# Kernel tuning notes

Hardware: AMD Instinct MI355X
Metric: run time of the kernel (lower is better)

## Reference

```python
import jax, jax.numpy as jnp
import numpy as np

N_EMBD = 768
N_HEAD = 12
HEAD_DIM = N_EMBD // N_HEAD


def setup_inputs() -> dict:
    key = jax.random.key(0)
    k1, k2, k3 = jax.random.split(key, 3)
    x = jax.random.normal(k1, (2, 2048, N_EMBD), dtype=jnp.float32)
    # Dense kernels (no bias), scaled like Glorot-ish init
    w_qkv = jax.random.normal(k2, (N_EMBD, 3 * N_EMBD), dtype=jnp.float32) * (1.0 / np.sqrt(N_EMBD))
    w_proj = jax.random.normal(k3, (N_EMBD, N_EMBD), dtype=jnp.float32) * (1.0 / np.sqrt(N_EMBD))
    return {"x": x, "w_qkv": w_qkv, "w_proj": w_proj}


def reference(x, w_qkv, w_proj):
    b, t, _ = x.shape
    qkv = x @ w_qkv                                  # [b, t, 3*n_embd]
    q, k, v = jnp.split(qkv, 3, axis=-1)
    def split_heads(z):
        return z.reshape(b, t, N_HEAD, HEAD_DIM).transpose(0, 2, 1, 3)  # [b, h, t, d]
    q, k, v = split_heads(q), split_heads(k), split_heads(v)
    scale = jnp.float32(HEAD_DIM) ** -0.5
    att = jnp.einsum('bhqd,bhkd->bhqk', q, k) * scale  # [b, h, t, t]
    # lower-triangular causal mask, additive -1e9 on masked (future) positions
    mask = jnp.tril(jnp.ones((t, t), dtype=jnp.float32))
    att = att + (1.0 - mask)[None, None, :, :] * jnp.float32(-1e9)
    att = jax.nn.softmax(att, axis=-1)
    out = jnp.einsum('bhqk,bhkd->bhqd', att, v)      # [b, h, t, d]
    out = out.transpose(0, 2, 1, 3).reshape(b, t, N_EMBD)
    return out @ w_proj
```

## Files before the change

kernel.cpp:

```cpp
#include <hip/hip_runtime.h>

#define T_SEQ   2048
#define EMBD    768
#define N_HEAD  12
#define HDIM    64
#define BATCH   2

typedef float f32x4 __attribute__((ext_vector_type(4)));
typedef short bf16x8 __attribute__((ext_vector_type(8)));
typedef unsigned short u16;
typedef unsigned int u32;
typedef u16 u16x4 __attribute__((ext_vector_type(4)));

#define MFMA_BF16(a, b, c) __builtin_amdgcn_mfma_f32_16x16x32_bf16((a), (b), (c), 0, 0, 0)

__device__ __forceinline__ u16 f2bf(float f) {
    union { float f; unsigned u; } v; v.f = f;
    unsigned r = v.u + 0x7fffu + ((v.u >> 16) & 1u);
    return (u16)(r >> 16);
}

__device__ __forceinline__ u32 pack2(float hi, float lo) {
    union { float f; u32 u; } a, b;
    a.f = hi; b.f = lo;
    return __builtin_amdgcn_perm(a.u, b.u, 0x07060302u);
}

__device__ __forceinline__ void gload_lds16(const u16* g, u16* l) {
    __builtin_amdgcn_global_load_lds(
        (const __attribute__((address_space(1))) u32*)g,
        (__attribute__((address_space(3))) u32*)l, 16, 0, 0);
}

__global__ __launch_bounds__(256) void prep_kernel(
    const float* __restrict__ x, const float* __restrict__ wq,
    const float* __restrict__ wp, u16* __restrict__ xb,
    u16* __restrict__ wqT, u16* __restrict__ wpT)
{
    const int bid = blockIdx.x;
    const int tid = threadIdx.x;
    if (bid < 1536) {
        const int i = bid * 2048 + tid * 8;
        const float4 f0 = *(const float4*)&x[i];
        const float4 f1 = *(const float4*)&x[i + 4];
        bf16x8 r;
        r[0] = (short)f2bf(f0.x); r[1] = (short)f2bf(f0.y);
        r[2] = (short)f2bf(f0.z); r[3] = (short)f2bf(f0.w);
        r[4] = (short)f2bf(f1.x); r[5] = (short)f2bf(f1.y);
        r[6] = (short)f2bf(f1.z); r[7] = (short)f2bf(f1.w);
        *(bf16x8*)&xb[i] = r;
        return;
    }
    __shared__ float tile[32][33];
    const float* W; u16* Wt; int N, t;
    if (bid < 3264) { W = wq; Wt = wqT; N = 2304; t = bid - 1536; }
    else            { W = wp; Wt = wpT; N = 768;  t = bid - 3264; }
    const int ntiles = N / 32;
    const int n0 = (t % ntiles) * 32;
    const int k0 = (t / ntiles) * 32;
    const int c  = tid & 31;
    const int r8 = tid >> 5;
#pragma unroll
    for (int rr = r8; rr < 32; rr += 8)
        tile[rr][c] = W[(size_t)(k0 + rr) * N + n0 + c];
    __syncthreads();
#pragma unroll
    for (int rr = r8; rr < 32; rr += 8)
        Wt[(size_t)(n0 + rr) * 768 + k0 + c] = f2bf(tile[c][rr]);
}

template <int NCOLS, int SCATTER>
__global__ __launch_bounds__(256, 2) void mfma_gemm(
    const u16* __restrict__ A, const u16* __restrict__ Bt,
    float* __restrict__ C, u16* __restrict__ Qo, u16* __restrict__ Ko,
    u16* __restrict__ Vo)
{
    __shared__ u16 As[128 * 64];
    __shared__ u16 Bs[128 * 64];
    const int tid  = threadIdx.x;
    const int lane = tid & 63, wave = tid >> 6;
    const int l15  = lane & 15, quad = lane >> 4;
    const int wy   = wave >> 1, wx = wave & 1;
    const int row0 = blockIdx.y * 128, col0 = blockIdx.x * 128;

    const int sr = lane >> 3;
    const int sc = lane & 7;
    const int g  = sc ^ sr;
    const u16* gA[4]; const u16* gB[4]; u16* lA[4]; u16* lB[4];
#pragma unroll
    for (int i = 0; i < 4; ++i) {
        const int rb = (i * 4 + wave) * 8;
        gA[i] = &A [(size_t)(row0 + rb + sr) * 768 + g * 8];
        gB[i] = &Bt[(size_t)(col0 + rb + sr) * 768 + g * 8];
        lA[i] = &As[rb * 64];
        lB[i] = &Bs[rb * 64];
    }

    f32x4 acc[4][4];
#pragma unroll
    for (int i = 0; i < 4; ++i)
#pragma unroll
        for (int j = 0; j < 4; ++j) acc[i][j] = (f32x4){0.f, 0.f, 0.f, 0.f};

    for (int k0 = 0; k0 < 768; k0 += 64) {
        __syncthreads();
#pragma unroll
        for (int i = 0; i < 4; ++i) gload_lds16(gA[i] + k0, lA[i]);
#pragma unroll
        for (int i = 0; i < 4; ++i) gload_lds16(gB[i] + k0, lB[i]);
        __syncthreads();
        bf16x8 af[4][2], bfr[4][2];
#pragma unroll
        for (int ks = 0; ks < 2; ++ks) {
#pragma unroll
            for (int mt = 0; mt < 4; ++mt)
                af[mt][ks] = *(const bf16x8*)&As[(wy * 64 + mt * 16 + l15) * 64 +
                                                 (((ks * 4 + quad) ^ (l15 & 7)) * 8)];
#pragma unroll
            for (int nt = 0; nt < 4; ++nt)
                bfr[nt][ks] = *(const bf16x8*)&Bs[(wx * 64 + nt * 16 + l15) * 64 +
                                                  (((ks * 4 + quad) ^ (l15 & 7)) * 8)];
        }
#pragma unroll
        for (int ks = 0; ks < 2; ++ks)
#pragma unroll
            for (int mt = 0; mt < 4; ++mt)
#pragma unroll
                for (int nt = 0; nt < 4; ++nt)
                    acc[mt][nt] = MFMA_BF16(af[mt][ks], bfr[nt][ks], acc[mt][nt]);
    }

    const float qscale = 0.18033688f;
#pragma unroll
    for (int mt = 0; mt < 4; ++mt) {
#pragma unroll
        for (int nt = 0; nt < 4; ++nt) {
            const int col = col0 + wx * 64 + nt * 16 + l15;
            if (SCATTER) {
                const int which = col / 768;
                const int hh = (col - which * 768) >> 6;
                const int dd = col & 63;
                if (which == 2) {
                    const int row = row0 + wy * 64 + mt * 16 + quad * 4;
                    const int bb = row >> 11, t0 = row & 2047;
                    u16x4 pk;
#pragma unroll
                    for (int r = 0; r < 4; ++r) pk[r] = f2bf(acc[mt][nt][r]);
                    *(u16x4*)&Vo[((size_t)(bb * N_HEAD + hh) * HDIM + dd) * T_SEQ + t0] = pk;
                } else {
                    u16* dst = (which == 0) ? Qo : Ko;
                    const float sc2 = (which == 0) ? qscale : 1.0f;
                    const size_t hb = (size_t)hh * T_SEQ * HDIM + dd;
#pragma unroll
                    for (int r = 0; r < 4; ++r) {
                        const int row = row0 + wy * 64 + mt * 16 + quad * 4 + r;
                        const int bb = row >> 11, tt = row & 2047;
                        dst[(size_t)bb * N_HEAD * T_SEQ * HDIM + hb + (size_t)tt * HDIM] =
                            f2bf(acc[mt][nt][r] * sc2);
                    }
                }
            } else {
#pragma unroll
                for (int r = 0; r < 4; ++r) {
                    const int row = row0 + wy * 64 + mt * 16 + quad * 4 + r;
                    C[(size_t)row * NCOLS + col] = acc[mt][nt][r];
                }
            }
        }
    }
}

__global__ __launch_bounds__(256, 3) void attn_mfma(
    const u16* __restrict__ Q, const u16* __restrict__ K,
    const u16* __restrict__ Vt, u16* __restrict__ Aout)
{
    __shared__ float Comb[5120];
    u16* PsAll = (u16*)Comb;

    const int tid  = threadIdx.x;
    const int lane = tid & 63, wave = tid >> 6;
    const int l15  = lane & 15, quad = lane >> 4;

    const int f    = blockIdx.x;
    const int slot = f >> 3;
    const int bh   = (f & 7) * 3 + (slot >> 5);
    const int p    = slot & 31;
    const int b    = bh / N_HEAD, h = bh - b * N_HEAD;

    const int j      = (wave < 2) ? (63 - p) : p;
    const int parity = wave & 1;
    const int qb     = j * 32;
    const int nk     = (j >> 1) + 1;
    const size_t base = (size_t)bh * T_SEQ * HDIM;

    bf16x8 qf[2][2];
#pragma unroll
    for (int jq = 0; jq < 2; ++jq)
#pragma unroll
        for (int ks = 0; ks < 2; ++ks)
            qf[jq][ks] = *(const bf16x8*)&Q[base + (size_t)(qb + jq * 16 + l15) * HDIM +
                                            ks * 32 + quad * 8];

    f32x4 o[2][4], l_acc[2];
#pragma unroll
    for (int jq = 0; jq < 2; ++jq) {
        l_acc[jq] = (f32x4){0.f, 0.f, 0.f, 0.f};
#pragma unroll
        for (int nt = 0; nt < 4; ++nt) o[jq][nt] = (f32x4){0.f, 0.f, 0.f, 0.f};
    }

    bf16x8 onesf;
#pragma unroll
    for (int u = 0; u < 8; ++u) onesf[u] = (short)0x3F80;

    u16* myPs = PsAll + wave * 2304;

    for (int kt = parity; kt < nk; kt += 2) {
        const int k0 = kt * 64;

        f32x4 s[4][2];
#pragma unroll
        for (int i = 0; i < 4; ++i)
#pragma unroll
            for (int jq = 0; jq < 2; ++jq) s[i][jq] = (f32x4){0.f, 0.f, 0.f, 0.f};
#pragma unroll
        for (int ks = 0; ks < 2; ++ks) {
            bf16x8 kf[4];
#pragma unroll
            for (int i = 0; i < 4; ++i)
                kf[i] = *(const bf16x8*)&K[base + (size_t)(k0 + i * 16 + l15) * HDIM +
                                           ks * 32 + quad * 8];
#pragma unroll
            for (int i = 0; i < 4; ++i)
#pragma unroll
                for (int jq = 0; jq < 2; ++jq)
                    s[i][jq] = MFMA_BF16(kf[i], qf[jq][ks], s[i][jq]);
        }

        bf16x8 vf[4][2];
#pragma unroll
        for (int nt = 0; nt < 4; ++nt)
#pragma unroll
            for (int ks = 0; ks < 2; ++ks)
                vf[nt][ks] = *(const bf16x8*)&Vt[base + (size_t)(nt * 16 + l15) * T_SEQ +
                                                 k0 + ks * 32 + quad * 8];

#pragma unroll
        for (int i = 0; i < 2; ++i)
#pragma unroll
            for (int jq = 0; jq < 2; ++jq) {
                float pv[4];
                if (k0 + i * 16 + 15 > qb + jq * 16) {
                    const int q = qb + jq * 16 + l15;
#pragma unroll
                    for (int r = 0; r < 4; ++r) {
                        const int key = k0 + i * 16 + quad * 4 + r;
                        pv[r] = exp2f((key > q) ? -1e30f : s[i][jq][r]);
                    }
                } else {
#pragma unroll
                    for (int r = 0; r < 4; ++r) pv[r] = exp2f(s[i][jq][r]);
                }
                uint2 w;
                w.x = pack2(pv[1], pv[0]);
                w.y = pack2(pv[3], pv[2]);
                *(uint2*)&myPs[(jq * 16 + l15) * 72 + i * 16 + quad * 4] = w;
            }

        bf16x8 pa0[2];
#pragma unroll
        for (int jq = 0; jq < 2; ++jq)
            pa0[jq] = *(const bf16x8*)&myPs[(jq * 16 + l15) * 72 + quad * 8];

#pragma unroll
        for (int i = 2; i < 4; ++i)
#pragma unroll
            for (int jq = 0; jq < 2; ++jq) {
                float pv[4];
                if (k0 + i * 16 + 15 > qb + jq * 16) {
                    const int q = qb + jq * 16 + l15;
#pragma unroll
                    for (int r = 0; r < 4; ++r) {
                        const int key = k0 + i * 16 + quad * 4 + r;
                        pv[r] = exp2f((key > q) ? -1e30f : s[i][jq][r]);
                    }
                } else {
#pragma unroll
                    for (int r = 0; r < 4; ++r) pv[r] = exp2f(s[i][jq][r]);
                }
                uint2 w;
                w.x = pack2(pv[1], pv[0]);
                w.y = pack2(pv[3], pv[2]);
                *(uint2*)&myPs[(jq * 16 + l15) * 72 + i * 16 + quad * 4] = w;
            }

#pragma unroll
        for (int jq = 0; jq < 2; ++jq) {
#pragma unroll
            for (int nt = 0; nt < 4; ++nt)
                o[jq][nt] = MFMA_BF16(pa0[jq], vf[nt][0], o[jq][nt]);
            l_acc[jq] = MFMA_BF16(pa0[jq], onesf, l_acc[jq]);
        }

        bf16x8 pa1[2];
#pragma unroll
        for (int jq = 0; jq < 2; ++jq)
            pa1[jq] = *(const bf16x8*)&myPs[(jq * 16 + l15) * 72 + 32 + quad * 8];
#pragma unroll
        for (int jq = 0; jq < 2; ++jq) {
#pragma unroll
            for (int nt = 0; nt < 4; ++nt)
                o[jq][nt] = MFMA_BF16(pa1[jq], vf[nt][1], o[jq][nt]);
            l_acc[jq] = MFMA_BF16(pa1[jq], onesf, l_acc[jq]);
        }
    }

    __syncthreads();
    if (parity == 1) {
        float* R = Comb + (wave >> 1) * 2560;
#pragma unroll
        for (int jq = 0; jq < 2; ++jq) {
#pragma unroll
            for (int nt = 0; nt < 4; ++nt)
#pragma unroll
                for (int r = 0; r < 4; ++r)
                    R[(jq * 16 + nt * 4 + r) * 64 + lane] = o[jq][nt][r];
#pragma unroll
            for (int r = 0; r < 4; ++r)
                R[(32 + jq * 4 + r) * 64 + lane] = l_acc[jq][r];
        }
    }
    __syncthreads();
    if (parity == 0) {
        const float* R = Comb + (wave >> 1) * 2560;
#pragma unroll
        for (int jq = 0; jq < 2; ++jq) {
#pragma unroll
            for (int nt = 0; nt < 4; ++nt)
#pragma unroll
                for (int r = 0; r < 4; ++r)
                    o[jq][nt][r] += R[(jq * 16 + nt * 4 + r) * 64 + lane];
#pragma unroll
            for (int r = 0; r < 4; ++r)
                l_acc[jq][r] += R[(32 + jq * 4 + r) * 64 + lane];
        }
#pragma unroll
        for (int jq = 0; jq < 2; ++jq) {
            f32x4 inv;
#pragma unroll
            for (int r = 0; r < 4; ++r) inv[r] = 1.0f / l_acc[jq][r];
#pragma unroll
            for (int nt = 0; nt < 4; ++nt) {
                const int d = nt * 16 + l15;
#pragma unroll
                for (int r = 0; r < 4; ++r) {
                    const int q = qb + jq * 16 + quad * 4 + r;
                    Aout[(size_t)(b * T_SEQ + q) * EMBD + h * HDIM + d] =
                        f2bf(o[jq][nt][r] * inv[r]);
                }
            }
        }
    }
}

extern "C" void kernel_launch(void* const* d_in, const int* in_sizes, int n_in,
                              void* d_out, int out_size, void* d_ws, size_t ws_size,
                              hipStream_t stream)
{
    (void)in_sizes; (void)n_in; (void)out_size; (void)ws_size;
    const float* x      = (const float*)d_in[0];
    const float* w_qkv  = (const float*)d_in[1];
    const float* w_proj = (const float*)d_in[2];
    float* out = (float*)d_out;

    u16* ws = (u16*)d_ws;
    const size_t NX  = (size_t)BATCH * T_SEQ * EMBD;
    const size_t NWQ = (size_t)EMBD * 3 * EMBD;
    const size_t NWP = (size_t)EMBD * EMBD;
    const size_t SZ  = (size_t)BATCH * N_HEAD * T_SEQ * HDIM;
    u16* xb     = ws;
    u16* wqkvT  = xb + NX;
    u16* wprojT = wqkvT + NWQ;
    u16* Qb     = wprojT + NWP;
    u16* Kb     = Qb + SZ;
    u16* Vtb    = Kb + SZ;
    u16* Ab     = Vtb + SZ;

    dim3 blk(256);
    prep_kernel<<<dim3(3840), blk, 0, stream>>>(x, w_qkv, w_proj, xb, wqkvT, wprojT);

    mfma_gemm<3 * EMBD, 1><<<dim3(3 * EMBD / 128, BATCH * T_SEQ / 128), blk, 0, stream>>>(
        xb, wqkvT, nullptr, Qb, Kb, Vtb);

    attn_mfma<<<dim3(32 * N_HEAD * BATCH), blk, 0, stream>>>(Qb, Kb, Vtb, Ab);

    mfma_gemm<EMBD, 0><<<dim3(EMBD / 128, BATCH * T_SEQ / 128), blk, 0, stream>>>(
        Ab, wprojT, out, nullptr, nullptr, nullptr);
}
```

Before: 163.8 us.

## Prefetch K fragments in attention and use smaller M tile for projection GEMM

```diff
diff --git a/kernel.cpp b/kernel.cpp
--- a/kernel.cpp
+++ b/kernel.cpp
@@ -69,70 +69,74 @@
         Wt[(size_t)(n0 + rr) * 768 + k0 + c] = f2bf(tile[c][rr]);
 }
 
-template <int NCOLS, int SCATTER>
-__global__ __launch_bounds__(256, 2) void mfma_gemm(
+template <int NCOLS, int SCATTER, int TM>
+__global__ __launch_bounds__(256, 3) void mfma_gemm(
     const u16* __restrict__ A, const u16* __restrict__ Bt,
     float* __restrict__ C, u16* __restrict__ Qo, u16* __restrict__ Ko,
     u16* __restrict__ Vo)
 {
-    __shared__ u16 As[128 * 64];
+    constexpr int MT = TM / 32;
+    constexpr int AI = TM / 32;
+    __shared__ u16 As[TM * 64];
     __shared__ u16 Bs[128 * 64];
     const int tid  = threadIdx.x;
     const int lane = tid & 63, wave = tid >> 6;
     const int l15  = lane & 15, quad = lane >> 4;
     const int wy   = wave >> 1, wx = wave & 1;
-    const int row0 = blockIdx.y * 128, col0 = blockIdx.x * 128;
+    const int row0 = blockIdx.y * TM, col0 = blockIdx.x * 128;
 
     const int sr = lane >> 3;
     const int sc = lane & 7;
     const int g  = sc ^ sr;
-    const u16* gA[4]; const u16* gB[4]; u16* lA[4]; u16* lB[4];
+    const u16* gA[AI]; const u16* gB[4]; u16* lA[AI]; u16* lB[4];
+#pragma unroll
+    for (int i = 0; i < AI; ++i) {
+        const int rb = (i * 4 + wave) * 8;
+        gA[i] = &A[(size_t)(row0 + rb + sr) * 768 + g * 8];
+        lA[i] = &As[rb * 64];
+    }
 #pragma unroll
     for (int i = 0; i < 4; ++i) {
         const int rb = (i * 4 + wave) * 8;
-        gA[i] = &A [(size_t)(row0 + rb + sr) * 768 + g * 8];
         gB[i] = &Bt[(size_t)(col0 + rb + sr) * 768 + g * 8];
-        lA[i] = &As[rb * 64];
         lB[i] = &Bs[rb * 64];
     }
 
-    f32x4 acc[4][4];
-#pragma unroll
-    for (int i = 0; i < 4; ++i)
+    f32x4 acc[MT][4];
+#pragma unroll
+    for (int i = 0; i < MT; ++i)
 #pragma unroll
         for (int j = 0; j < 4; ++j) acc[i][j] = (f32x4){0.f, 0.f, 0.f, 0.f};
 
     for (int k0 = 0; k0 < 768; k0 += 64) {
         __syncthreads();
 #pragma unroll
-        for (int i = 0; i < 4; ++i) gload_lds16(gA[i] + k0, lA[i]);
+        for (int i = 0; i < AI; ++i) gload_lds16(gA[i] + k0, lA[i]);
 #pragma unroll
         for (int i = 0; i < 4; ++i) gload_lds16(gB[i] + k0, lB[i]);
         __syncthreads();
-        bf16x8 af[4][2], bfr[4][2];
 #pragma unroll
         for (int ks = 0; ks < 2; ++ks) {
-#pragma unroll
-            for (int mt = 0; mt < 4; ++mt)
-                af[mt][ks] = *(const bf16x8*)&As[(wy * 64 + mt * 16 + l15) * 64 +
-                                                 (((ks * 4 + quad) ^ (l15 & 7)) * 8)];
+            bf16x8 af[MT], bfr[4];
+#pragma unroll
+            for (int mt = 0; mt < MT; ++mt)
+                af[mt] = *(const bf16x8*)&As[(wy * (TM / 2) + mt * 16 + l15) * 64 +
+                                             (((ks * 4 + quad) ^ (l15 & 7)) * 8)];
 #pragma unroll
             for (int nt = 0; nt < 4; ++nt)
-                bfr[nt][ks] = *(const bf16x8*)&Bs[(wx * 64 + nt * 16 + l15) * 64 +
-                                                  (((ks * 4 + quad) ^ (l15 & 7)) * 8)];
-        }
-#pragma unroll
-        for (int ks = 0; ks < 2; ++ks)
-#pragma unroll
-            for (int mt = 0; mt < 4; ++mt)
+                bfr[nt] = *(const bf16x8*)&Bs[(wx * 64 + nt * 16 + l15) * 64 +
+                                              (((ks * 4 + quad) ^ (l15 & 7)) * 8)];
+#pragma unroll
+            for (int mt = 0; mt < MT; ++mt)
 #pragma unroll
                 for (int nt = 0; nt < 4; ++nt)
-                    acc[mt][nt] = MFMA_BF16(af[mt][ks], bfr[nt][ks], acc[mt][nt]);
+                    acc[mt][nt] = MFMA_BF16(af[mt], bfr[nt], acc[mt][nt]);
+        }
     }
 
     const float qscale = 0.18033688f;
 #pragma unroll
-    for (int mt = 0; mt < 4; ++mt) {
+    for (int mt = 0; mt < MT; ++mt) {
 #pragma unroll
         for (int nt = 0; nt < 4; ++nt) {
             const int col = col0 + wx * 64 + nt * 16 + l15;
@@ -141,7 +145,7 @@
                 const int hh = (col - which * 768) >> 6;
                 const int dd = col & 63;
                 if (which == 2) {
-                    const int row = row0 + wy * 64 + mt * 16 + quad * 4;
+                    const int row = row0 + wy * (TM / 2) + mt * 16 + quad * 4;
                     const int bb = row >> 11, t0 = row & 2047;
                     u16x4 pk;
 #pragma unroll
@@ -153,7 +157,7 @@
                     const size_t hb = (size_t)hh * T_SEQ * HDIM + dd;
 #pragma unroll
                     for (int r = 0; r < 4; ++r) {
-                        const int row = row0 + wy * 64 + mt * 16 + quad * 4 + r;
+                        const int row = row0 + wy * (TM / 2) + mt * 16 + quad * 4 + r;
                         const int bb = row >> 11, tt = row & 2047;
                         dst[(size_t)bb * N_HEAD * T_SEQ * HDIM + hb + (size_t)tt * HDIM] =
                             f2bf(acc[mt][nt][r] * sc2);
@@ -162,7 +166,7 @@
             } else {
 #pragma unroll
                 for (int r = 0; r < 4; ++r) {
-                    const int row = row0 + wy * 64 + mt * 16 + quad * 4 + r;
+                    const int row = row0 + wy * (TM / 2) + mt * 16 + quad * 4 + r;
                     C[(size_t)row * NCOLS + col] = acc[mt][nt][r];
                 }
             }
@@ -215,8 +219,20 @@
 
     u16* myPs = PsAll + wave * 2304;
 
+    bf16x8 kc[4][2];
+    {
+        const int k0 = parity * 64;
+#pragma unroll
+        for (int i = 0; i < 4; ++i)
+#pragma unroll
+            for (int ks = 0; ks < 2; ++ks)
+                kc[i][ks] = *(const bf16x8*)&K[base + (size_t)(k0 + i * 16 + l15) * HDIM +
+                                               ks * 32 + quad * 8];
+    }
+
     for (int kt = parity; kt < nk; kt += 2) {
         const int k0 = kt * 64;
+        const bool pf = (kt + 2 < nk);
 
         f32x4 s[4][2];
 #pragma unroll
@@ -224,26 +240,18 @@
 #pragma unroll
             for (int jq = 0; jq < 2; ++jq) s[i][jq] = (f32x4){0.f, 0.f, 0.f, 0.f};
 #pragma unroll
-        for (int ks = 0; ks < 2; ++ks) {
-            bf16x8 kf[4];
-#pragma unroll
-            for (int i = 0; i < 4; ++i)
-                kf[i] = *(const bf16x8*)&K[base + (size_t)(k0 + i * 16 + l15) * HDIM +
-                                           ks * 32 + quad * 8];
-#pragma unroll
-            for (int i = 0; i < 4; ++i)
+        for (int ks = 0; ks < 2; ++ks)
+#pragma unroll
+            for (int i = 0; i < 2; ++i)
 #pragma unroll
                 for (int jq = 0; jq < 2; ++jq)
-                    s[i][jq] = MFMA_BF16(kf[i], qf[jq][ks], s[i][jq]);
-        }
-
-        bf16x8 vf[4][2];
+                    s[i][jq] = MFMA_BF16(kc[i][ks], qf[jq][ks], s[i][jq]);
+
+        bf16x8 vf0[4];
 #pragma unroll
         for (int nt = 0; nt < 4; ++nt)
-#pragma unroll
-            for (int ks = 0; ks < 2; ++ks)
-                vf[nt][ks] = *(const bf16x8*)&Vt[base + (size_t)(nt * 16 + l15) * T_SEQ +
-                                                 k0 + ks * 32 + quad * 8];
+            vf0[nt] = *(const bf16x8*)&Vt[base + (size_t)(nt * 16 + l15) * T_SEQ +
+                                          k0 + quad * 8];
 
 #pragma unroll
         for (int i = 0; i < 2; ++i)
@@ -267,6 +275,24 @@
                 *(uint2*)&myPs[(jq * 16 + l15) * 72 + i * 16 + quad * 4] = w;
             }
 
+#pragma unroll
+        for (int ks = 0; ks < 2; ++ks)
+#pragma unroll
+            for (int i = 2; i < 4; ++i)
+#pragma unroll
+                for (int jq = 0; jq < 2; ++jq)
+                    s[i][jq] = MFMA_BF16(kc[i][ks], qf[jq][ks], s[i][jq]);
+
+        if (pf) {
+            const int kn0 = k0 + 128;
+#pragma unroll
+            for (int i = 0; i < 4; ++i)
+#pragma unroll
+                for (int ks = 0; ks < 2; ++ks)
+                    kc[i][ks] = *(const bf16x8*)&K[base +
+                        (size_t)(kn0 + i * 16 + l15) * HDIM + ks * 32 + quad * 8];
+        }
+
         bf16x8 pa0[2];
 #pragma unroll
         for (int jq = 0; jq < 2; ++jq)
@@ -298,10 +324,15 @@
         for (int jq = 0; jq < 2; ++jq) {
 #pragma unroll
             for (int nt = 0; nt < 4; ++nt)
-                o[jq][nt] = MFMA_BF16(pa0[jq], vf[nt][0], o[jq][nt]);
+                o[jq][nt] = MFMA_BF16(pa0[jq], vf0[nt], o[jq][nt]);
             l_acc[jq] = MFMA_BF16(pa0[jq], onesf, l_acc[jq]);
         }
 
+        bf16x8 vf1[4];
+#pragma unroll
+        for (int nt = 0; nt < 4; ++nt)
+            vf1[nt] = *(const bf16x8*)&Vt[base + (size_t)(nt * 16 + l15) * T_SEQ +
+                                          k0 + 32 + quad * 8];
         bf16x8 pa1[2];
 #pragma unroll
         for (int jq = 0; jq < 2; ++jq)
@@ -310,7 +341,7 @@
         for (int jq = 0; jq < 2; ++jq) {
 #pragma unroll
             for (int nt = 0; nt < 4; ++nt)
-                o[jq][nt] = MFMA_BF16(pa1[jq], vf[nt][1], o[jq][nt]);
+                o[jq][nt] = MFMA_BF16(pa1[jq], vf1[nt], o[jq][nt]);
             l_acc[jq] = MFMA_BF16(pa1[jq], onesf, l_acc[jq]);
         }
     }
@@ -389,11 +420,11 @@
     dim3 blk(256);
     prep_kernel<<<dim3(3840), blk, 0, stream>>>(x, w_qkv, w_proj, xb, wqkvT, wprojT);
 
-    mfma_gemm<3 * EMBD, 1><<<dim3(3 * EMBD / 128, BATCH * T_SEQ / 128), blk, 0, stream>>>(
+    mfma_gemm<3 * EMBD, 1, 128><<<dim3(3 * EMBD / 128, BATCH * T_SEQ / 128), blk, 0, stream>>>(
         xb, wqkvT, nullptr, Qb, Kb, Vtb);
 
     attn_mfma<<<dim3(32 * N_HEAD * BATCH), blk, 0, stream>>>(Qb, Kb, Vtb, Ab);
 
-    mfma_gemm<EMBD, 0><<<dim3(EMBD / 128, BATCH * T_SEQ / 128), blk, 0, stream>>>(
+    mfma_gemm<EMBD, 0, 64><<<dim3(EMBD / 128, BATCH * T_SEQ / 64), blk, 0, stream>>>(
         Ab, wprojT, out, nullptr, nullptr, nullptr);
 }
```

Result: no change. 164.4 us (+0.4%).
